# Performance work log

Hardware: AMD Instinct MI355X
Metric: run time of the kernel (lower is better)

The kernel has to match this reference:

```python
import jax, jax.numpy as jnp
import numpy as np

THRESH = 0.1
BN_EPS = 1e-5
B, N, C_IN, C_HID, C_OUT = 4096, 128, 64, 256, 128


def setup_inputs() -> dict:
    key = jax.random.key(0)
    ks = jax.random.split(key, 10)
    a = jax.random.uniform(ks[0], (B, N, N), dtype=jnp.float32)
    v = jax.random.normal(ks[1], (B, N, C_IN), dtype=jnp.float32)
    # MLP params: Linear(C_IN->C_HID) + BN + ReLU + Linear(C_HID->C_OUT) + BN + ReLU
    W1 = jax.random.normal(ks[2], (C_IN, C_HID), dtype=jnp.float32) / np.sqrt(C_IN)
    b1 = jnp.zeros((C_HID,), jnp.float32)
    g1 = 1.0 + 0.1 * jax.random.normal(ks[3], (C_HID,), dtype=jnp.float32)
    be1 = 0.1 * jax.random.normal(ks[4], (C_HID,), dtype=jnp.float32)
    rm1 = 0.1 * jax.random.normal(ks[5], (C_HID,), dtype=jnp.float32)
    rv1 = jnp.ones((C_HID,), jnp.float32)
    W2 = jax.random.normal(ks[6], (C_HID, C_OUT), dtype=jnp.float32) / np.sqrt(C_HID)
    b2 = jnp.zeros((C_OUT,), jnp.float32)
    g2 = 1.0 + 0.1 * jax.random.normal(ks[7], (C_OUT,), dtype=jnp.float32)
    be2 = 0.1 * jax.random.normal(ks[8], (C_OUT,), dtype=jnp.float32)
    rm2 = 0.1 * jax.random.normal(ks[9], (C_OUT,), dtype=jnp.float32)
    rv2 = jnp.ones((C_OUT,), jnp.float32)
    return {"a": a, "v": v, "W1": W1, "b1": b1, "g1": g1, "be1": be1, "rm1": rm1, "rv1": rv1,
            "W2": W2, "b2": b2, "g2": g2, "be2": be2, "rm2": rm2, "rv2": rv2}


def reference(a, v, W1, b1, g1, be1, rm1, rv1, W2, b2, g2, be2, rm2, rv2):
    # threshold adjacency
    a_th = (a >= THRESH).astype(v.dtype)            # [B, N, N]
    # D^-0.5 A D^-0.5 as row/col rescaling (equivalent to diag_embed + bmm)
    d_inv_sqrt = jnp.sum(a_th, axis=-1) ** -0.5     # [B, N]
    a_bar = d_inv_sqrt[:, :, None] * a_th * d_inv_sqrt[:, None, :]
    # propagate
    h = jnp.einsum('bnm,bmc->bnc', a_bar, v)        # [B, N, C_IN]
    x = h.reshape(-1, h.shape[-1])                  # [(B N), C_IN]
    # MLP with BatchNorm in eval mode (running stats), dropout is identity in eval
    x = x @ W1 + b1
    x = (x - rm1) * jax.lax.rsqrt(rv1 + BN_EPS) * g1 + be1
    x = jax.nn.relu(x)
    x = x @ W2 + b2
    x = (x - rm2) * jax.lax.rsqrt(rv2 + BN_EPS) * g2 + be2
    x = jax.nn.relu(x)
    return x
```

## Files before the change

kernel.cpp:

```cpp
#include <hip/hip_runtime.h>


#define THRESH 0.1f
#define BN_EPS 1e-5f

typedef __attribute__((ext_vector_type(8))) short bf16x8;
typedef __attribute__((ext_vector_type(4))) float f32x4;

__device__ __forceinline__ unsigned short f2bf(float f) {
    union { float f; unsigned u; } x; x.f = f;
    unsigned r = x.u + 0x7FFFu + ((x.u >> 16) & 1u);
    return (unsigned short)(r >> 16);
}

__device__ __forceinline__ unsigned cvt_pk(float lo, float hi) {
    unsigned r;
    asm("v_cvt_pk_bf16_f32 %0, %1, %2" : "=v"(r) : "v"(lo), "v"(hi));
    return r;
}

__global__ void gcn_prep(const float* __restrict__ W1, const float* __restrict__ b1,
                         const float* __restrict__ g1, const float* __restrict__ be1,
                         const float* __restrict__ rm1, const float* __restrict__ rv1,
                         const float* __restrict__ W2, const float* __restrict__ b2,
                         const float* __restrict__ g2, const float* __restrict__ be2,
                         const float* __restrict__ rm2, const float* __restrict__ rv2,
                         unsigned short* __restrict__ W1s, unsigned short* __restrict__ W2s,
                         float* __restrict__ sh1, float* __restrict__ sh2) {
    int t = blockIdx.x * blockDim.x + threadIdx.x;
    if (t < 256 * 64) {
        int n = t >> 6, kp = t & 63;
        int sp = kp >> 3, lo = kp & 7;
        int s  = sp ^ (n & 7);
        int k2 = s * 8 + lo;
        int r = k2 & 3, aa = (k2 >> 2) & 1, gg = (k2 >> 3) & 3, T = k2 >> 5;
        int k = T * 32 + aa * 16 + gg * 4 + r;
        float sc = g1[n] * rsqrtf(rv1[n] + BN_EPS);
        W1s[t] = f2bf(W1[k * 256 + n] * sc);
    }
    {
        int n = t >> 8, kp = t & 255;
        int sp = kp >> 3, lo = kp & 7;
        int s  = sp ^ (n & 7);
        int k2 = s * 8 + lo;
        int r = k2 & 3, aa = (k2 >> 2) & 1, gg = (k2 >> 3) & 3, T = k2 >> 5;
        int k = T * 32 + aa * 16 + gg * 4 + r;
        float sc = g2[n] * rsqrtf(rv2[n] + BN_EPS);
        W2s[t] = f2bf(W2[k * 128 + n] * sc);
    }
    if (t < 256) {
        float s = g1[t] * rsqrtf(rv1[t] + BN_EPS);
        sh1[t] = (b1[t] - rm1[t]) * s + be1[t];
    }
    if (t < 128) {
        float s = g2[t] * rsqrtf(rv2[t] + BN_EPS);
        sh2[t] = (b2[t] - rm2[t]) * s + be2[t];
    }
}

__global__ void __launch_bounds__(256, 5)
gcn_prop(const float* __restrict__ A, const float* __restrict__ V,
         unsigned short* __restrict__ hP) {
    __shared__ unsigned short s_vtt[64 * 136];

    const int t    = threadIdx.x;
    const int lane = t & 63;
    const int w    = t >> 6;
    const int r16  = lane & 15;
    const int g    = lane >> 4;
    const int b    = blockIdx.x;

    const int mloc  = lane & 31;
    const int chalf = (lane >> 5) * 32;
    const float* vb = V + (size_t)b * 8192 + (size_t)(32 * w + mloc) * 64 + chalf;
    f32x4 pv[8];
#pragma unroll
    for (int q = 0; q < 8; ++q) pv[q] = *(const f32x4*)(vb + 4 * q);

    const float* ab = A + (size_t)b * 16384 + (size_t)(32 * w + r16) * 128;
    bf16x8 afrag[2][4];
    int cnt0 = 0, cnt1 = 0;
#pragma unroll
    for (int mt = 0; mt < 2; ++mt)
#pragma unroll
        for (int ks = 0; ks < 4; ++ks) {
            const float* p = ab + mt * 2048 + ks * 32 + 8 * g;
            f32x4 x0 = *(const f32x4*)p;
            f32x4 x1 = *(const f32x4*)(p + 4);
            union { unsigned short s[8]; bf16x8 v; } u;
            u.s[0] = (x0.x >= THRESH) ? (unsigned short)0x3F80u : (unsigned short)0u;
            u.s[1] = (x0.y >= THRESH) ? (unsigned short)0x3F80u : (unsigned short)0u;
            u.s[2] = (x0.z >= THRESH) ? (unsigned short)0x3F80u : (unsigned short)0u;
            u.s[3] = (x0.w >= THRESH) ? (unsigned short)0x3F80u : (unsigned short)0u;
            u.s[4] = (x1.x >= THRESH) ? (unsigned short)0x3F80u : (unsigned short)0u;
            u.s[5] = (x1.y >= THRESH) ? (unsigned short)0x3F80u : (unsigned short)0u;
            u.s[6] = (x1.z >= THRESH) ? (unsigned short)0x3F80u : (unsigned short)0u;
            u.s[7] = (x1.w >= THRESH) ? (unsigned short)0x3F80u : (unsigned short)0u;
            afrag[mt][ks] = u.v;
            int c = (x0.x >= THRESH) + (x0.y >= THRESH) + (x0.z >= THRESH) + (x0.w >= THRESH)
                  + (x1.x >= THRESH) + (x1.y >= THRESH) + (x1.z >= THRESH) + (x1.w >= THRESH);
            if (mt == 0) cnt0 += c; else cnt1 += c;
        }
    cnt0 += __shfl_xor(cnt0, 16); cnt0 += __shfl_xor(cnt0, 32);
    cnt1 += __shfl_xor(cnt1, 16); cnt1 += __shfl_xor(cnt1, 32);
    const float dinv0 = rsqrtf((float)cnt0);
    const float dinv1 = rsqrtf((float)cnt1);

    {
        float dm = (lane & 16) ? dinv1 : dinv0;
        int m = 32 * w + mloc;
#pragma unroll
        for (int q = 0; q < 8; ++q) {
            int c = chalf + 4 * q;
            s_vtt[(c + 0) * 136 + m] = f2bf(pv[q].x * dm);
            s_vtt[(c + 1) * 136 + m] = f2bf(pv[q].y * dm);
            s_vtt[(c + 2) * 136 + m] = f2bf(pv[q].z * dm);
            s_vtt[(c + 3) * 136 + m] = f2bf(pv[q].w * dm);
        }
    }
    __syncthreads();

    f32x4 acc1[4][2];
#pragma unroll
    for (int ct = 0; ct < 4; ++ct)
#pragma unroll
        for (int mt = 0; mt < 2; ++mt) acc1[ct][mt] = f32x4{0.f, 0.f, 0.f, 0.f};
#pragma unroll
    for (int ks = 0; ks < 4; ++ks)
#pragma unroll
        for (int ct = 0; ct < 4; ++ct) {
            bf16x8 av = *(const bf16x8*)(s_vtt + (ct * 16 + r16) * 136 + ks * 32 + 8 * g);
            acc1[ct][0] = __builtin_amdgcn_mfma_f32_16x16x32_bf16(av, afrag[0][ks], acc1[ct][0], 0, 0, 0);
            acc1[ct][1] = __builtin_amdgcn_mfma_f32_16x16x32_bf16(av, afrag[1][ks], acc1[ct][1], 0, 0, 0);
        }

#pragma unroll
    for (int mt = 0; mt < 2; ++mt) {
        float d = (mt == 0) ? dinv0 : dinv1;
        size_t m = (size_t)(b * 128 + 32 * w + 16 * mt + r16);
#pragma unroll
        for (int ks2 = 0; ks2 < 2; ++ks2) {
            union { unsigned u[4]; bf16x8 v; } pk;
            pk.u[0] = cvt_pk(acc1[2 * ks2][mt][0] * d,     acc1[2 * ks2][mt][1] * d);
            pk.u[1] = cvt_pk(acc1[2 * ks2][mt][2] * d,     acc1[2 * ks2][mt][3] * d);
            pk.u[2] = cvt_pk(acc1[2 * ks2 + 1][mt][0] * d, acc1[2 * ks2 + 1][mt][1] * d);
            pk.u[3] = cvt_pk(acc1[2 * ks2 + 1][mt][2] * d, acc1[2 * ks2 + 1][mt][3] * d);
            *(bf16x8*)(hP + m * 64 + ks2 * 32 + 8 * g) = pk.v;
        }
    }
}

__global__ void __launch_bounds__(512, 2)
gcn_mlp(const unsigned short* __restrict__ hP,
        const unsigned short* __restrict__ W1s, const unsigned short* __restrict__ W2s,
        const float* __restrict__ sh1g, const float* __restrict__ sh2g,
        float* __restrict__ out) {
    __shared__ char smem[99840];
    unsigned short* W1L = (unsigned short*)smem;
    unsigned short* W2L = (unsigned short*)(smem + 32768);
    float* s_sh1 = (float*)(smem + 98304);
    float* s_sh2 = (float*)(smem + 99328);

    const int t    = threadIdx.x;
    const int lane = t & 63;
    const int w    = t >> 6;
    const int r16  = lane & 15;
    const int g    = lane >> 4;
    const int rg   = w & 1;
    const int ch   = w >> 1;

#pragma unroll
    for (int q = 0; q < 4; ++q)
        *(f32x4*)(smem + t * 64 + q * 16) = *(const f32x4*)((const char*)W1s + t * 64 + q * 16);
#pragma unroll
    for (int q = 0; q < 8; ++q)
        *(f32x4*)(smem + 32768 + t * 128 + q * 16) =
            *(const f32x4*)((const char*)W2s + t * 128 + q * 16);
    if (t < 256) s_sh1[t] = sh1g[t];
    if (t < 128) s_sh2[t] = sh2g[t];
    __syncthreads();

    const size_t tile0 = (size_t)blockIdx.x * 8;

    bf16x8 nb[4][2];
    {
        size_t mb = tile0 * 128 + rg * 64;
#pragma unroll
        for (int mt = 0; mt < 4; ++mt)
#pragma unroll
            for (int ks2 = 0; ks2 < 2; ++ks2)
                nb[mt][ks2] = *(const bf16x8*)(hP + (mb + 16 * mt + r16) * 64 + ks2 * 32 + 8 * g);
    }

#pragma unroll 1
    for (int i = 0; i < 8; ++i) {
        bf16x8 bh[4][2];
#pragma unroll
        for (int mt = 0; mt < 4; ++mt)
#pragma unroll
            for (int ks2 = 0; ks2 < 2; ++ks2) bh[mt][ks2] = nb[mt][ks2];

        if (i < 7) {
            size_t mb = (tile0 + i + 1) * 128 + rg * 64;
#pragma unroll
            for (int mt = 0; mt < 4; ++mt)
#pragma unroll
                for (int ks2 = 0; ks2 < 2; ++ks2)
                    nb[mt][ks2] = *(const bf16x8*)(hP + (mb + 16 * mt + r16) * 64 + ks2 * 32 + 8 * g);
        }

        f32x4 acc3[4][2];
#pragma unroll
        for (int mt = 0; mt < 4; ++mt)
#pragma unroll
            for (int q = 0; q < 2; ++q) acc3[mt][q] = f32x4{0.f, 0.f, 0.f, 0.f};

#pragma unroll
        for (int T = 0; T < 8; ++T) {
            f32x4 a2[4][2];
#pragma unroll
            for (int mt = 0; mt < 4; ++mt)
#pragma unroll
                for (int ctp = 0; ctp < 2; ++ctp) a2[mt][ctp] = f32x4{0.f, 0.f, 0.f, 0.f};
#pragma unroll
            for (int ctp = 0; ctp < 2; ++ctp) {
                int ct = 2 * T + ctp;
                int n  = ct * 16 + r16;
#pragma unroll
                for (int ks2 = 0; ks2 < 2; ++ks2) {
                    int sp = (ks2 * 4 + g) ^ (n & 7);
                    bf16x8 aw = *(const bf16x8*)(W1L + n * 64 + sp * 8);
#pragma unroll
                    for (int mt = 0; mt < 4; ++mt)
                        a2[mt][ctp] = __builtin_amdgcn_mfma_f32_16x16x32_bf16(aw, bh[mt][ks2], a2[mt][ctp], 0, 0, 0);
                }
            }
            unsigned wds[4][4];
#pragma unroll
            for (int ctp = 0; ctp < 2; ++ctp) {
                f32x4 sh = *(const f32x4*)(s_sh1 + (2 * T + ctp) * 16 + 4 * g);
#pragma unroll
                for (int mt = 0; mt < 4; ++mt) {
                    float y0 = fmaxf(a2[mt][ctp][0] + sh.x, 0.f);
                    float y1 = fmaxf(a2[mt][ctp][1] + sh.y, 0.f);
                    float y2 = fmaxf(a2[mt][ctp][2] + sh.z, 0.f);
                    float y3 = fmaxf(a2[mt][ctp][3] + sh.w, 0.f);
                    wds[mt][2 * ctp + 0] = cvt_pk(y0, y1);
                    wds[mt][2 * ctp + 1] = cvt_pk(y2, y3);
                }
            }
#pragma unroll
            for (int q = 0; q < 2; ++q) {
                int ct3 = ch * 2 + q;
                int n   = ct3 * 16 + r16;
                int sp  = (T * 4 + g) ^ (n & 7);
                bf16x8 bw = *(const bf16x8*)(W2L + n * 256 + sp * 8);
#pragma unroll
                for (int mt = 0; mt < 4; ++mt) {
                    union { unsigned u[4]; bf16x8 v; } af;
                    af.u[0] = wds[mt][0]; af.u[1] = wds[mt][1];
                    af.u[2] = wds[mt][2]; af.u[3] = wds[mt][3];
                    acc3[mt][q] = __builtin_amdgcn_mfma_f32_16x16x32_bf16(af.v, bw, acc3[mt][q], 0, 0, 0);
                }
            }
        }

        float* ob = out + ((tile0 + i) * 128 + rg * 64) * 128;
#pragma unroll
        for (int q = 0; q < 2; ++q) {
            int c = (ch * 2 + q) * 16 + r16;
            float sh = s_sh2[c];
#pragma unroll
            for (int mt = 0; mt < 4; ++mt)
#pragma unroll
                for (int r = 0; r < 4; ++r) {
                    int row = 16 * mt + 4 * g + r;
                    ob[row * 128 + c] = fmaxf(acc3[mt][q][r] + sh, 0.f);
                }
        }
    }
}

extern "C" void kernel_launch(void* const* d_in, const int* in_sizes, int n_in,
                              void* d_out, int out_size, void* d_ws, size_t ws_size,
                              hipStream_t stream) {
    (void)in_sizes; (void)n_in; (void)out_size; (void)ws_size;
    const float* a   = (const float*)d_in[0];
    const float* v   = (const float*)d_in[1];
    const float* W1  = (const float*)d_in[2];
    const float* b1  = (const float*)d_in[3];
    const float* g1  = (const float*)d_in[4];
    const float* be1 = (const float*)d_in[5];
    const float* rm1 = (const float*)d_in[6];
    const float* rv1 = (const float*)d_in[7];
    const float* W2  = (const float*)d_in[8];
    const float* b2  = (const float*)d_in[9];
    const float* g2  = (const float*)d_in[10];
    const float* be2 = (const float*)d_in[11];
    const float* rm2 = (const float*)d_in[12];
    const float* rv2 = (const float*)d_in[13];

    char* ws = (char*)d_ws;
    unsigned short* W1s = (unsigned short*)ws;
    unsigned short* W2s = (unsigned short*)(ws + 32768);
    float* sh1 = (float*)(ws + 98304);
    float* sh2 = (float*)(ws + 99328);
    unsigned short* hP = (unsigned short*)(ws + 102400);

    gcn_prep<<<128, 256, 0, stream>>>(W1, b1, g1, be1, rm1, rv1,
                                      W2, b2, g2, be2, rm2, rv2,
                                      W1s, W2s, sh1, sh2);
    gcn_prop<<<4096, 256, 0, stream>>>(a, v, hP);
    gcn_mlp<<<512, 512, 0, stream>>>(hP, W1s, W2s, sh1, sh2, (float*)d_out);
}
```

Before: 228.6 us.

## Repartition MLP waves by rows to eliminate redundant hidden-layer computation

Each wave now owns 32 rows and all 128 output columns instead of 64 rows and a 32-column slice of the output. Previously every wave recomputed the full 256-wide hidden activation for its rows, duplicating the first GEMM four times across column groups. The new split computes each hidden value once per block. In exchange each wave reads all of W2 from LDS and holds more accumulator registers, which may raise register pressure.

```diff
diff --git a/kernel.cpp b/kernel.cpp
--- a/kernel.cpp
+++ b/kernel.cpp
@@ -166,8 +166,6 @@
     const int w    = t >> 6;
     const int r16  = lane & 15;
     const int g    = lane >> 4;
-    const int rg   = w & 1;
-    const int ch   = w >> 1;
 
 #pragma unroll
     for (int q = 0; q < 4; ++q)
@@ -180,67 +178,65 @@
     if (t < 128) s_sh2[t] = sh2g[t];
     __syncthreads();
 
-    const size_t tile0 = (size_t)blockIdx.x * 8;
-
-    bf16x8 nb[4][2];
+    const size_t row00 = (size_t)blockIdx.x * 1024;
+
+    bf16x8 nb[2][2];
     {
-        size_t mb = tile0 * 128 + rg * 64;
-#pragma unroll
-        for (int mt = 0; mt < 4; ++mt)
+        size_t mb = row00 + 32 * w;
+#pragma unroll
+        for (int mt = 0; mt < 2; ++mt)
 #pragma unroll
             for (int ks2 = 0; ks2 < 2; ++ks2)
                 nb[mt][ks2] = *(const bf16x8*)(hP + (mb + 16 * mt + r16) * 64 + ks2 * 32 + 8 * g);
     }
 
 #pragma unroll 1
-    for (int i = 0; i < 8; ++i) {
-        bf16x8 bh[4][2];
-#pragma unroll
-        for (int mt = 0; mt < 4; ++mt)
+    for (int i = 0; i < 4; ++i) {
+        bf16x8 bh[2][2];
+#pragma unroll
+        for (int mt = 0; mt < 2; ++mt)
 #pragma unroll
             for (int ks2 = 0; ks2 < 2; ++ks2) bh[mt][ks2] = nb[mt][ks2];
 
-        if (i < 7) {
-            size_t mb = (tile0 + i + 1) * 128 + rg * 64;
-#pragma unroll
-            for (int mt = 0; mt < 4; ++mt)
+        if (i < 3) {
+            size_t mb = row00 + (i + 1) * 256 + 32 * w;
+#pragma unroll
+            for (int mt = 0; mt < 2; ++mt)
 #pragma unroll
                 for (int ks2 = 0; ks2 < 2; ++ks2)
                     nb[mt][ks2] = *(const bf16x8*)(hP + (mb + 16 * mt + r16) * 64 + ks2 * 32 + 8 * g);
         }
 
-        f32x4 acc3[4][2];
-#pragma unroll
-        for (int mt = 0; mt < 4; ++mt)
-#pragma unroll
-            for (int q = 0; q < 2; ++q) acc3[mt][q] = f32x4{0.f, 0.f, 0.f, 0.f};
+        f32x4 acc3[2][8];
+#pragma unroll
+        for (int mt = 0; mt < 2; ++mt)
+#pragma unroll
+            for (int ct = 0; ct < 8; ++ct) acc3[mt][ct] = f32x4{0.f, 0.f, 0.f, 0.f};
 
 #pragma unroll
         for (int T = 0; T < 8; ++T) {
-            f32x4 a2[4][2];
-#pragma unroll
-            for (int mt = 0; mt < 4; ++mt)
+            f32x4 a2[2][2];
+#pragma unroll
+            for (int mt = 0; mt < 2; ++mt)
 #pragma unroll
                 for (int ctp = 0; ctp < 2; ++ctp) a2[mt][ctp] = f32x4{0.f, 0.f, 0.f, 0.f};
 #pragma unroll
             for (int ctp = 0; ctp < 2; ++ctp) {
-                int ct = 2 * T + ctp;
-                int n  = ct * 16 + r16;
+                int n = (2 * T + ctp) * 16 + r16;
 #pragma unroll
                 for (int ks2 = 0; ks2 < 2; ++ks2) {
                     int sp = (ks2 * 4 + g) ^ (n & 7);
                     bf16x8 aw = *(const bf16x8*)(W1L + n * 64 + sp * 8);
-#pragma unroll
-                    for (int mt = 0; mt < 4; ++mt)
-                        a2[mt][ctp] = __builtin_amdgcn_mfma_f32_16x16x32_bf16(aw, bh[mt][ks2], a2[mt][ctp], 0, 0, 0);
+                    a2[0][ctp] = __builtin_amdgcn_mfma_f32_16x16x32_bf16(aw, bh[0][ks2], a2[0][ctp], 0, 0, 0);
+                    a2[1][ctp] = __builtin_amdgcn_mfma_f32_16x16x32_bf16(aw, bh[1][ks2], a2[1][ctp], 0, 0, 0);
                 }
             }
-            unsigned wds[4][4];
+            unsigned wds[2][4];
 #pragma unroll
             for (int ctp = 0; ctp < 2; ++ctp) {
                 f32x4 sh = *(const f32x4*)(s_sh1 + (2 * T + ctp) * 16 + 4 * g);
 #pragma unroll
-                for (int mt = 0; mt < 4; ++mt) {
+                for (int mt = 0; mt < 2; ++mt) {
                     float y0 = fmaxf(a2[mt][ctp][0] + sh.x, 0.f);
                     float y1 = fmaxf(a2[mt][ctp][1] + sh.y, 0.f);
                     float y2 = fmaxf(a2[mt][ctp][2] + sh.z, 0.f);
@@ -250,32 +246,31 @@
                 }
             }
 #pragma unroll
-            for (int q = 0; q < 2; ++q) {
-                int ct3 = ch * 2 + q;
-                int n   = ct3 * 16 + r16;
-                int sp  = (T * 4 + g) ^ (n & 7);
+            for (int ct3 = 0; ct3 < 8; ++ct3) {
+                int n  = ct3 * 16 + r16;
+                int sp = (T * 4 + g) ^ (n & 7);
                 bf16x8 bw = *(const bf16x8*)(W2L + n * 256 + sp * 8);
 #pragma unroll
-                for (int mt = 0; mt < 4; ++mt) {
+                for (int mt = 0; mt < 2; ++mt) {
                     union { unsigned u[4]; bf16x8 v; } af;
                     af.u[0] = wds[mt][0]; af.u[1] = wds[mt][1];
                     af.u[2] = wds[mt][2]; af.u[3] = wds[mt][3];
-                    acc3[mt][q] = __builtin_amdgcn_mfma_f32_16x16x32_bf16(af.v, bw, acc3[mt][q], 0, 0, 0);
+                    acc3[mt][ct3] = __builtin_amdgcn_mfma_f32_16x16x32_bf16(af.v, bw, acc3[mt][ct3], 0, 0, 0);
                 }
             }
         }
 
-        float* ob = out + ((tile0 + i) * 128 + rg * 64) * 128;
-#pragma unroll
-        for (int q = 0; q < 2; ++q) {
-            int c = (ch * 2 + q) * 16 + r16;
+        float* ob = out + (row00 + i * 256 + 32 * w) * 128;
+#pragma unroll
+        for (int ct3 = 0; ct3 < 8; ++ct3) {
+            int c = ct3 * 16 + r16;
             float sh = s_sh2[c];
 #pragma unroll
-            for (int mt = 0; mt < 4; ++mt)
+            for (int mt = 0; mt < 2; ++mt)
 #pragma unroll
                 for (int r = 0; r < 4; ++r) {
                     int row = 16 * mt + 4 * g + r;
-                    ob[row * 128 + c] = fmaxf(acc3[mt][q][r] + sh, 0.f);
+                    ob[row * 128 + c] = fmaxf(acc3[mt][ct3][r] + sh, 0.f);
                 }
         }
     }
```

Measured after the change: 227.0 us. No clear change (-0.7%).
